# Performance work log

Measured on AMD Instinct MI355X. Metric: run time of the kernel, lower is better.

The kernel has to match this reference:

```python
import jax, jax.numpy as jnp
import numpy as np

K = 7  # kernel_size


def _patches(x, k):
    # x: [N, C, H, W] -> [K*K, N, C, H, W]; zero-padded local windows in
    # torch.nn.functional.unfold order (kernel positions row-major).
    N, C, H, W = x.shape
    p = k // 2
    xp = jnp.pad(x, ((0, 0), (0, 0), (p, p), (p, p)))
    return jnp.stack([xp[:, :, i:i + H, j:j + W]
                      for i in range(k) for j in range(k)], axis=0)


def setup_inputs() -> dict:
    key = jax.random.key(0)
    k1, k2 = jax.random.split(key)
    x = jax.random.normal(k1, (4, 128, 80, 80), dtype=jnp.float32)
    feat_in = jax.random.normal(k2, (4, 128, 80, 80), dtype=jnp.float32)
    return {"x": x, "feat_in": feat_in}


def reference(x, feat_in):
    N, C, H, W = feat_in.shape
    k2 = K * K
    # theta_x == phi_x == x in the original module.
    phi_p = _patches(x, K)                            # [K2, N, Cq, H, W]
    # local dot products: weight[k, n, h, w] = sum_c phi_window * theta_center
    w = jnp.einsum('knchw,nchw->knhw', phi_p, x)      # [K2, N, H, W]
    # L1-style normalization over the window (plain sum, as in the source)
    w = w / jnp.sum(w, axis=0, keepdims=True)
    feat_p = _patches(feat_in, K)                     # [K2, N, C, H, W]
    out = jnp.einsum('knhw,knchw->nchw', w, feat_p)   # [N, C, H, W]
    pairwise_weight = w.transpose(1, 2, 3, 0).reshape(N * H * W, 1, k2)
    return out, pairwise_weight
```

## Files before the change

kernel.cpp:

```cpp
#include <hip/hip_runtime.h>


namespace {

constexpr int CN = 4, CC = 128, HT = 80, WD = 80;
constexpr int KK = 7, K2 = 49, PD = 3;
constexpr int TW = 16, TH = 4;
constexpr int HW_ = TW + 6;
constexpr int HH_ = TH + 6;
constexpr int HENT = HW_ * HH_;
constexpr int HCHUNK = (HENT * 4 + 63) / 64;
constexpr int HPADF = HCHUNK * 64;
constexpr int PLANE = HT * WD;
constexpr int GSTRIDE = 4 * PLANE;
constexpr int OUT_ELEMS = CN * CC * PLANE;
constexpr int NW = 4;
constexpr int GPW = 8;
constexpr int WR = 53;

__device__ __forceinline__ void make_off(int* off, int bx, int by, int lane) {
#pragma unroll
  for (int q = 0; q < HCHUNK; ++q) {
    int f = q * 64 + lane;
    int e = f >> 2;
    if (e > HENT - 1) e = HENT - 1;
    const int ch = f & 3;
    const int r  = e / HW_;
    const int cl = e - r * HW_;
    int gh = by * TH - PD + r;
    gh = gh < 0 ? 0 : (gh > HT - 1 ? HT - 1 : gh);
    int gw = bx * TW - PD + cl;
    gw = gw < 0 ? 0 : (gw > WD - 1 ? WD - 1 : gw);
    off[q] = ch * PLANE + gh * WD + gw;
  }
}

__device__ __forceinline__ void issue_chunks(const float* gbase, const int* off,
                                             float* lds) {
#if __has_builtin(__builtin_amdgcn_global_load_lds)
#pragma unroll
  for (int q = 0; q < HCHUNK; ++q) {
    __builtin_amdgcn_global_load_lds(
        (const __attribute__((address_space(1))) void*)(gbase + off[q]),
        (__attribute__((address_space(3))) void*)(lds + q * 64), 4, 0, 0);
  }
#else
  const int lane = (int)(threadIdx.x & 63);
#pragma unroll
  for (int q = 0; q < HCHUNK; ++q) lds[q * 64 + lane] = gbase[off[q]];
  asm volatile("s_waitcnt lgkmcnt(0)" ::: "memory");
#endif
}

#define WAIT_VM(n_lit)                                      \
  asm volatile("s_waitcnt vmcnt(" #n_lit ")" ::: "memory"); \
  __builtin_amdgcn_sched_barrier(0)

__global__ __launch_bounds__(256) void lnl2d_fused4(
    const float* __restrict__ x, const float* __restrict__ feat,
    float* __restrict__ dout) {
  __shared__ float halo[NW * 3][HPADF];
  __shared__ float wred[64][WR];
  __shared__ float inv[64];

  const int tid  = (int)threadIdx.x;
  const int wv   = tid >> 6;
  const int lane = tid & 63;
  const int tx = lane & (TW - 1), ty = lane >> 4;
  const int bx = (int)blockIdx.x, by = (int)blockIdx.y, n = (int)blockIdx.z;
  const int h = by * TH + ty, w = bx * TW + tx;

  const float* xw = x + (size_t)n * CC * PLANE + (size_t)wv * 32 * PLANE;
  const float* fw = feat + (size_t)n * CC * PLANE + (size_t)wv * 32 * PLANE;
  float* out = dout;
  float* pw  = dout + OUT_ELEMS;

  int off[HCHUNK];
  make_off(off, bx, by, lane);

#pragma unroll
  for (int i = 0; i < (64 * WR + 255) / 256; ++i) {
    const int idx = i * 256 + tid;
    if (idx < 64 * WR) ((float*)wred)[idx] = 0.f;
  }
  __syncthreads();

  float acc[K2];
#pragma unroll
  for (int k = 0; k < K2; ++k) acc[k] = 0.f;

  float* hb0 = halo[wv * 3 + 0];
  float* hb1 = halo[wv * 3 + 1];
  float* hb2 = halo[wv * 3 + 2];

  issue_chunks(xw, off, hb0);
  issue_chunks(xw + GSTRIDE, off, hb1);
  int goff = 2 * GSTRIDE;
#pragma unroll
  for (int g = 0; g < GPW; ++g) {
    if (g < GPW - 2) {
      float* dst = (g % 3 == 0) ? hb2 : ((g % 3 == 1) ? hb0 : hb1);
      issue_chunks(xw + goff, off, dst);
      goff += GSTRIDE;
    }
    if (g < GPW - 2)      { WAIT_VM(28); }
    else if (g == GPW - 2){ WAIT_VM(14); }
    else                  { WAIT_VM(0); }
    const float* hb = (g % 3 == 0) ? hb0 : ((g % 3 == 1) ? hb1 : hb2);
    const float4 c4 = *(const float4*)(hb + ((ty + PD) * HW_ + (tx + PD)) * 4);
#pragma unroll
    for (int di = 0; di < KK; ++di)
#pragma unroll
      for (int dj = 0; dj < KK; ++dj) {
        const float4 n4 = *(const float4*)(hb + ((ty + di) * HW_ + (tx + dj)) * 4);
        acc[di * KK + dj] += c4.x * n4.x + c4.y * n4.y + c4.z * n4.z + c4.w * n4.w;
      }
  }

#pragma unroll
  for (int di = 0; di < KK; ++di)
#pragma unroll
    for (int dj = 0; dj < KK; ++dj) {
      const int hh = h + di - PD, ww = w + dj - PD;
      if ((unsigned)hh >= (unsigned)HT || (unsigned)ww >= (unsigned)WD)
        acc[di * KK + dj] = 0.f;
    }
#pragma unroll
  for (int k = 0; k < K2; ++k) atomicAdd(&wred[lane][k], acc[k]);

  __syncthreads();

  issue_chunks(fw, off, hb0);
  issue_chunks(fw + GSTRIDE, off, hb1);

  float wk[K2];
  float ssum = 0.f;
#pragma unroll
  for (int k = 0; k < K2; ++k) { wk[k] = wred[lane][k]; ssum += wk[k]; }
  const float invs = 1.0f / ssum;
#pragma unroll
  for (int k = 0; k < K2; ++k) wk[k] *= invs;
  if (wv == 0) inv[lane] = invs;

  float4 ov[GPW];
#pragma unroll
  for (int g = 0; g < GPW; ++g) ov[g] = make_float4(0.f, 0.f, 0.f, 0.f);

  goff = 2 * GSTRIDE;
#pragma unroll
  for (int g = 0; g < GPW; ++g) {
    if (g < GPW - 2) {
      float* dst = (g % 3 == 0) ? hb2 : ((g % 3 == 1) ? hb0 : hb1);
      issue_chunks(fw + goff, off, dst);
      goff += GSTRIDE;
    }
    if (g < GPW - 2)      { WAIT_VM(28); }
    else if (g == GPW - 2){ WAIT_VM(14); }
    else                  { WAIT_VM(0); }
    const float* hb = (g % 3 == 0) ? hb0 : ((g % 3 == 1) ? hb1 : hb2);
#pragma unroll
    for (int di = 0; di < KK; ++di)
#pragma unroll
      for (int dj = 0; dj < KK; ++dj) {
        const float4 n4 = *(const float4*)(hb + ((ty + di) * HW_ + (tx + dj)) * 4);
        const float f = wk[di * KK + dj];
        ov[g].x += f * n4.x; ov[g].y += f * n4.y; ov[g].z += f * n4.z; ov[g].w += f * n4.w;
      }
  }

  const size_t ob = (size_t)n * CC * PLANE + (size_t)wv * 32 * PLANE +
                    (size_t)(h * WD + w);
#pragma unroll
  for (int g = 0; g < GPW; ++g) {
    out[ob + (size_t)(4 * g + 0) * PLANE] = ov[g].x;
    out[ob + (size_t)(4 * g + 1) * PLANE] = ov[g].y;
    out[ob + (size_t)(4 * g + 2) * PLANE] = ov[g].z;
    out[ob + (size_t)(4 * g + 3) * PLANE] = ov[g].w;
  }

  __syncthreads();

#pragma unroll
  for (int r = 0; r < TH; ++r) {
    float* seg = pw + (size_t)(n * PLANE + (by * TH + r) * WD + bx * TW) * K2;
#pragma unroll
    for (int i = 0; i < (TW * K2) / 256; ++i) {
      const int idx = i * 256 + tid;
      const int col = idx / K2, k = idx - col * K2;
      seg[idx] = wred[r * TW + col][k] * inv[r * TW + col];
    }
    const int rem = TW * K2 - 256 * ((TW * K2) / 256);
    if (tid < rem) {
      const int idx = 256 * ((TW * K2) / 256) + tid;
      const int col = idx / K2, k = idx - col * K2;
      seg[idx] = wred[r * TW + col][k] * inv[r * TW + col];
    }
  }
}

}

extern "C" void kernel_launch(void* const* d_in, const int* in_sizes, int n_in,
                              void* d_out, int out_size, void* d_ws, size_t ws_size,
                              hipStream_t stream) {
  const float* x    = (const float*)d_in[0];
  const float* feat = (const float*)d_in[1];
  float* out        = (float*)d_out;
  dim3 grid(WD / TW, HT / TH, CN);
  lnl2d_fused4<<<grid, 256, 0, stream>>>(x, feat, out);
}
```

Measured before the change: 137.9 us.

## Split channels across eight waves with register-staged double-buffered halo loads

```diff
diff --git a/kernel.cpp b/kernel.cpp
--- a/kernel.cpp
+++ b/kernel.cpp
@@ -7,59 +7,18 @@
 constexpr int KK = 7, K2 = 49, PD = 3;
 constexpr int TW = 16, TH = 4;
 constexpr int HW_ = TW + 6;
-constexpr int HH_ = TH + 6;
-constexpr int HENT = HW_ * HH_;
-constexpr int HCHUNK = (HENT * 4 + 63) / 64;
-constexpr int HPADF = HCHUNK * 64;
+constexpr int HENT = 22 * 10;
 constexpr int PLANE = HT * WD;
 constexpr int GSTRIDE = 4 * PLANE;
 constexpr int OUT_ELEMS = CN * CC * PLANE;
-constexpr int NW = 4;
-constexpr int GPW = 8;
+constexpr int NW = 8;
+constexpr int GPW = 4;
 constexpr int WR = 53;
 
-__device__ __forceinline__ void make_off(int* off, int bx, int by, int lane) {
-#pragma unroll
-  for (int q = 0; q < HCHUNK; ++q) {
-    int f = q * 64 + lane;
-    int e = f >> 2;
-    if (e > HENT - 1) e = HENT - 1;
-    const int ch = f & 3;
-    const int r  = e / HW_;
-    const int cl = e - r * HW_;
-    int gh = by * TH - PD + r;
-    gh = gh < 0 ? 0 : (gh > HT - 1 ? HT - 1 : gh);
-    int gw = bx * TW - PD + cl;
-    gw = gw < 0 ? 0 : (gw > WD - 1 ? WD - 1 : gw);
-    off[q] = ch * PLANE + gh * WD + gw;
-  }
-}
-
-__device__ __forceinline__ void issue_chunks(const float* gbase, const int* off,
-                                             float* lds) {
-#if __has_builtin(__builtin_amdgcn_global_load_lds)
-#pragma unroll
-  for (int q = 0; q < HCHUNK; ++q) {
-    __builtin_amdgcn_global_load_lds(
-        (const __attribute__((address_space(1))) void*)(gbase + off[q]),
-        (__attribute__((address_space(3))) void*)(lds + q * 64), 4, 0, 0);
-  }
-#else
-  const int lane = (int)(threadIdx.x & 63);
-#pragma unroll
-  for (int q = 0; q < HCHUNK; ++q) lds[q * 64 + lane] = gbase[off[q]];
-  asm volatile("s_waitcnt lgkmcnt(0)" ::: "memory");
-#endif
-}
-
-#define WAIT_VM(n_lit)                                      \
-  asm volatile("s_waitcnt vmcnt(" #n_lit ")" ::: "memory"); \
-  __builtin_amdgcn_sched_barrier(0)
-
-__global__ __launch_bounds__(256) void lnl2d_fused4(
-    const float* __restrict__ x, const float* __restrict__ feat,
-    float* __restrict__ dout) {
-  __shared__ float halo[NW * 3][HPADF];
+__global__ __launch_bounds__(512) void lnl2d_v4(const float* __restrict__ x,
+                                                const float* __restrict__ feat,
+                                                float* __restrict__ dout) {
+  __shared__ float4 halo[NW][256];
   __shared__ float wred[64][WR];
   __shared__ float inv[64];
 
@@ -70,51 +29,71 @@
   const int bx = (int)blockIdx.x, by = (int)blockIdx.y, n = (int)blockIdx.z;
   const int h = by * TH + ty, w = bx * TW + tx;
 
-  const float* xw = x + (size_t)n * CC * PLANE + (size_t)wv * 32 * PLANE;
-  const float* fw = feat + (size_t)n * CC * PLANE + (size_t)wv * 32 * PLANE;
+  const float* xw = x + (size_t)n * CC * PLANE + (size_t)wv * 16 * PLANE;
+  const float* fw = feat + (size_t)n * CC * PLANE + (size_t)wv * 16 * PLANE;
   float* out = dout;
   float* pw  = dout + OUT_ELEMS;
 
-  int off[HCHUNK];
-  make_off(off, bx, by, lane);
+  int off4[4];
+  int eclamp[4];
+#pragma unroll
+  for (int c = 0; c < 4; ++c) {
+    int e = c * 64 + lane;
+    if (e > HENT - 1) e = HENT - 1;
+    eclamp[c] = e;
+    const int r = e / HW_, cl = e - r * HW_;
+    int gh = by * TH - PD + r;
+    gh = gh < 0 ? 0 : (gh > HT - 1 ? HT - 1 : gh);
+    int gw = bx * TW - PD + cl;
+    gw = gw < 0 ? 0 : (gw > WD - 1 ? WD - 1 : gw);
+    off4[c] = gh * WD + gw;
+  }
 
 #pragma unroll
-  for (int i = 0; i < (64 * WR + 255) / 256; ++i) {
-    const int idx = i * 256 + tid;
+  for (int i = 0; i < (64 * WR + 511) / 512; ++i) {
+    const int idx = i * 512 + tid;
     if (idx < 64 * WR) ((float*)wred)[idx] = 0.f;
   }
   __syncthreads();
+
+  auto ldg = [&](const float* gbase, float (&s)[16]) {
+#pragma unroll
+    for (int p = 0; p < 4; ++p) {
+      const float* bp = gbase + p * PLANE;
+#pragma unroll
+      for (int c = 0; c < 4; ++c) s[p * 4 + c] = bp[off4[c]];
+    }
+  };
+  auto stw = [&](const float (&s)[16]) {
+#pragma unroll
+    for (int c = 0; c < 4; ++c)
+      halo[wv][eclamp[c]] = make_float4(s[0 * 4 + c], s[1 * 4 + c],
+                                        s[2 * 4 + c], s[3 * 4 + c]);
+  };
 
   float acc[K2];
 #pragma unroll
   for (int k = 0; k < K2; ++k) acc[k] = 0.f;
 
-  float* hb0 = halo[wv * 3 + 0];
-  float* hb1 = halo[wv * 3 + 1];
-  float* hb2 = halo[wv * 3 + 2];
-
-  issue_chunks(xw, off, hb0);
-  issue_chunks(xw + GSTRIDE, off, hb1);
-  int goff = 2 * GSTRIDE;
-#pragma unroll
-  for (int g = 0; g < GPW; ++g) {
-    if (g < GPW - 2) {
-      float* dst = (g % 3 == 0) ? hb2 : ((g % 3 == 1) ? hb0 : hb1);
-      issue_chunks(xw + goff, off, dst);
-      goff += GSTRIDE;
-    }
-    if (g < GPW - 2)      { WAIT_VM(28); }
-    else if (g == GPW - 2){ WAIT_VM(14); }
-    else                  { WAIT_VM(0); }
-    const float* hb = (g % 3 == 0) ? hb0 : ((g % 3 == 1) ? hb1 : hb2);
-    const float4 c4 = *(const float4*)(hb + ((ty + PD) * HW_ + (tx + PD)) * 4);
+  auto corr = [&]() {
+    const float4 c4 = halo[wv][(ty + PD) * HW_ + (tx + PD)];
 #pragma unroll
     for (int di = 0; di < KK; ++di)
 #pragma unroll
       for (int dj = 0; dj < KK; ++dj) {
-        const float4 n4 = *(const float4*)(hb + ((ty + di) * HW_ + (tx + dj)) * 4);
+        const float4 n4 = halo[wv][(ty + di) * HW_ + (tx + dj)];
         acc[di * KK + dj] += c4.x * n4.x + c4.y * n4.y + c4.z * n4.z + c4.w * n4.w;
       }
+  };
+
+  {
+    float sA[16], sB[16];
+    ldg(xw + 0 * GSTRIDE, sA);
+    ldg(xw + 1 * GSTRIDE, sB);
+    stw(sA); ldg(xw + 2 * GSTRIDE, sA); corr();
+    stw(sB); ldg(xw + 3 * GSTRIDE, sB); corr();
+    stw(sA); corr();
+    stw(sB); corr();
   }
 
 #pragma unroll
@@ -130,8 +109,9 @@
 
   __syncthreads();
 
-  issue_chunks(fw, off, hb0);
-  issue_chunks(fw + GSTRIDE, off, hb1);
+  float sA[16], sB[16];
+  ldg(fw + 0 * GSTRIDE, sA);
+  ldg(fw + 1 * GSTRIDE, sB);
 
   float wk[K2];
   float ssum = 0.f;
@@ -146,29 +126,23 @@
 #pragma unroll
   for (int g = 0; g < GPW; ++g) ov[g] = make_float4(0.f, 0.f, 0.f, 0.f);
 
-  goff = 2 * GSTRIDE;
-#pragma unroll
-  for (int g = 0; g < GPW; ++g) {
-    if (g < GPW - 2) {
-      float* dst = (g % 3 == 0) ? hb2 : ((g % 3 == 1) ? hb0 : hb1);
-      issue_chunks(fw + goff, off, dst);
-      goff += GSTRIDE;
-    }
-    if (g < GPW - 2)      { WAIT_VM(28); }
-    else if (g == GPW - 2){ WAIT_VM(14); }
-    else                  { WAIT_VM(0); }
-    const float* hb = (g % 3 == 0) ? hb0 : ((g % 3 == 1) ? hb1 : hb2);
+  auto agg = [&](float4& o) {
 #pragma unroll
     for (int di = 0; di < KK; ++di)
 #pragma unroll
       for (int dj = 0; dj < KK; ++dj) {
-        const float4 n4 = *(const float4*)(hb + ((ty + di) * HW_ + (tx + dj)) * 4);
+        const float4 n4 = halo[wv][(ty + di) * HW_ + (tx + dj)];
         const float f = wk[di * KK + dj];
-        ov[g].x += f * n4.x; ov[g].y += f * n4.y; ov[g].z += f * n4.z; ov[g].w += f * n4.w;
+        o.x += f * n4.x; o.y += f * n4.y; o.z += f * n4.z; o.w += f * n4.w;
       }
-  }
+  };
 
-  const size_t ob = (size_t)n * CC * PLANE + (size_t)wv * 32 * PLANE +
+  stw(sA); ldg(fw + 2 * GSTRIDE, sA); agg(ov[0]);
+  stw(sB); ldg(fw + 3 * GSTRIDE, sB); agg(ov[1]);
+  stw(sA); agg(ov[2]);
+  stw(sB); agg(ov[3]);
+
+  const size_t ob = (size_t)n * CC * PLANE + (size_t)wv * 16 * PLANE +
                     (size_t)(h * WD + w);
 #pragma unroll
   for (int g = 0; g < GPW; ++g) {
@@ -183,17 +157,15 @@
 #pragma unroll
   for (int r = 0; r < TH; ++r) {
     float* seg = pw + (size_t)(n * PLANE + (by * TH + r) * WD + bx * TW) * K2;
-#pragma unroll
-    for (int i = 0; i < (TW * K2) / 256; ++i) {
-      const int idx = i * 256 + tid;
+    {
+      const int idx = tid;
       const int col = idx / K2, k = idx - col * K2;
       seg[idx] = wred[r * TW + col][k] * inv[r * TW + col];
     }
-    const int rem = TW * K2 - 256 * ((TW * K2) / 256);
-    if (tid < rem) {
-      const int idx = 256 * ((TW * K2) / 256) + tid;
-      const int col = idx / K2, k = idx - col * K2;
-      seg[idx] = wred[r * TW + col][k] * inv[r * TW + col];
+    const int idx2 = 512 + tid;
+    if (idx2 < TW * K2) {
+      const int col = idx2 / K2, k = idx2 - col * K2;
+      seg[idx2] = wred[r * TW + col][k] * inv[r * TW + col];
     }
   }
 }
@@ -207,5 +179,5 @@
   const float* feat = (const float*)d_in[1];
   float* out        = (float*)d_out;
   dim3 grid(WD / TW, HT / TH, CN);
-  lnl2d_fused4<<<grid, 256, 0, stream>>>(x, feat, out);
+  lnl2d_v4<<<grid, 512, 0, stream>>>(x, feat, out);
 }
```

Result: slower. 172.4 us (+25.0%).

## Deepen halo prefetch to four buffers and pad halo row stride

Applied to the files above, without the earlier changes.

```diff
diff --git a/kernel.cpp b/kernel.cpp
--- a/kernel.cpp
+++ b/kernel.cpp
@@ -6,16 +6,14 @@
 constexpr int CN = 4, CC = 128, HT = 80, WD = 80;
 constexpr int KK = 7, K2 = 49, PD = 3;
 constexpr int TW = 16, TH = 4;
-constexpr int HW_ = TW + 6;
-constexpr int HH_ = TH + 6;
-constexpr int HENT = HW_ * HH_;
+constexpr int HROW = 23;
+constexpr int HENT = 10 * HROW;
 constexpr int HCHUNK = (HENT * 4 + 63) / 64;
 constexpr int HPADF = HCHUNK * 64;
 constexpr int PLANE = HT * WD;
 constexpr int GSTRIDE = 4 * PLANE;
 constexpr int OUT_ELEMS = CN * CC * PLANE;
-constexpr int NW = 4;
-constexpr int GPW = 8;
+constexpr int NW = 4, GPW = 8;
 constexpr int WR = 53;
 
 __device__ __forceinline__ void make_off(int* off, int bx, int by, int lane) {
@@ -25,8 +23,8 @@
     int e = f >> 2;
     if (e > HENT - 1) e = HENT - 1;
     const int ch = f & 3;
-    const int r  = e / HW_;
-    const int cl = e - r * HW_;
+    const int r  = e / HROW;
+    const int cl = e - r * HROW;
     int gh = by * TH - PD + r;
     gh = gh < 0 ? 0 : (gh > HT - 1 ? HT - 1 : gh);
     int gw = bx * TW - PD + cl;
@@ -56,10 +54,10 @@
   asm volatile("s_waitcnt vmcnt(" #n_lit ")" ::: "memory"); \
   __builtin_amdgcn_sched_barrier(0)
 
-__global__ __launch_bounds__(256) void lnl2d_fused4(
-    const float* __restrict__ x, const float* __restrict__ feat,
-    float* __restrict__ dout) {
-  __shared__ float halo[NW * 3][HPADF];
+__global__ __launch_bounds__(256) void lnl2d_v6(const float* __restrict__ x,
+                                                const float* __restrict__ feat,
+                                                float* __restrict__ dout) {
+  __shared__ float halo[NW * 4][HPADF];
   __shared__ float wred[64][WR];
   __shared__ float inv[64];
 
@@ -85,36 +83,36 @@
   }
   __syncthreads();
 
+  float* hb[4] = {halo[wv * 4 + 0], halo[wv * 4 + 1], halo[wv * 4 + 2],
+                  halo[wv * 4 + 3]};
+
   float acc[K2];
 #pragma unroll
   for (int k = 0; k < K2; ++k) acc[k] = 0.f;
 
-  float* hb0 = halo[wv * 3 + 0];
-  float* hb1 = halo[wv * 3 + 1];
-  float* hb2 = halo[wv * 3 + 2];
-
-  issue_chunks(xw, off, hb0);
-  issue_chunks(xw + GSTRIDE, off, hb1);
-  int goff = 2 * GSTRIDE;
-#pragma unroll
-  for (int g = 0; g < GPW; ++g) {
-    if (g < GPW - 2) {
-      float* dst = (g % 3 == 0) ? hb2 : ((g % 3 == 1) ? hb0 : hb1);
-      issue_chunks(xw + goff, off, dst);
-      goff += GSTRIDE;
-    }
-    if (g < GPW - 2)      { WAIT_VM(28); }
-    else if (g == GPW - 2){ WAIT_VM(14); }
-    else                  { WAIT_VM(0); }
-    const float* hb = (g % 3 == 0) ? hb0 : ((g % 3 == 1) ? hb1 : hb2);
-    const float4 c4 = *(const float4*)(hb + ((ty + PD) * HW_ + (tx + PD)) * 4);
+  auto corr = [&](const float* b) {
+    const float4* h4 = (const float4*)b;
+    const float4 c4 = h4[(ty + PD) * HROW + tx + PD];
 #pragma unroll
     for (int di = 0; di < KK; ++di)
 #pragma unroll
       for (int dj = 0; dj < KK; ++dj) {
-        const float4 n4 = *(const float4*)(hb + ((ty + di) * HW_ + (tx + dj)) * 4);
+        const float4 n4 = h4[(ty + di) * HROW + tx + dj];
         acc[di * KK + dj] += c4.x * n4.x + c4.y * n4.y + c4.z * n4.z + c4.w * n4.w;
       }
+  };
+
+  issue_chunks(xw + 0 * GSTRIDE, off, hb[0]);
+  issue_chunks(xw + 1 * GSTRIDE, off, hb[1]);
+  issue_chunks(xw + 2 * GSTRIDE, off, hb[2]);
+#pragma unroll
+  for (int g = 0; g < GPW; ++g) {
+    if (g < GPW - 3) issue_chunks(xw + (g + 3) * GSTRIDE, off, hb[(g + 3) & 3]);
+    if (g < GPW - 3)      { WAIT_VM(45); }
+    else if (g == GPW - 3){ WAIT_VM(30); }
+    else if (g == GPW - 2){ WAIT_VM(15); }
+    else                  { WAIT_VM(0); }
+    corr(hb[g & 3]);
   }
 
 #pragma unroll
@@ -130,8 +128,9 @@
 
   __syncthreads();
 
-  issue_chunks(fw, off, hb0);
-  issue_chunks(fw + GSTRIDE, off, hb1);
+  issue_chunks(fw + 0 * GSTRIDE, off, hb[0]);
+  issue_chunks(fw + 1 * GSTRIDE, off, hb[1]);
+  issue_chunks(fw + 2 * GSTRIDE, off, hb[2]);
 
   float wk[K2];
   float ssum = 0.f;
@@ -146,23 +145,19 @@
 #pragma unroll
   for (int g = 0; g < GPW; ++g) ov[g] = make_float4(0.f, 0.f, 0.f, 0.f);
 
-  goff = 2 * GSTRIDE;
 #pragma unroll
   for (int g = 0; g < GPW; ++g) {
-    if (g < GPW - 2) {
-      float* dst = (g % 3 == 0) ? hb2 : ((g % 3 == 1) ? hb0 : hb1);
-      issue_chunks(fw + goff, off, dst);
-      goff += GSTRIDE;
-    }
-    if (g < GPW - 2)      { WAIT_VM(28); }
-    else if (g == GPW - 2){ WAIT_VM(14); }
+    if (g < GPW - 3) issue_chunks(fw + (g + 3) * GSTRIDE, off, hb[(g + 3) & 3]);
+    if (g < GPW - 3)      { WAIT_VM(45); }
+    else if (g == GPW - 3){ WAIT_VM(30); }
+    else if (g == GPW - 2){ WAIT_VM(15); }
     else                  { WAIT_VM(0); }
-    const float* hb = (g % 3 == 0) ? hb0 : ((g % 3 == 1) ? hb1 : hb2);
+    const float4* h4 = (const float4*)hb[g & 3];
 #pragma unroll
     for (int di = 0; di < KK; ++di)
 #pragma unroll
       for (int dj = 0; dj < KK; ++dj) {
-        const float4 n4 = *(const float4*)(hb + ((ty + di) * HW_ + (tx + dj)) * 4);
+        const float4 n4 = h4[(ty + di) * HROW + tx + dj];
         const float f = wk[di * KK + dj];
         ov[g].x += f * n4.x; ov[g].y += f * n4.y; ov[g].z += f * n4.z; ov[g].w += f * n4.w;
       }
@@ -207,5 +202,5 @@
   const float* feat = (const float*)d_in[1];
   float* out        = (float*)d_out;
   dim3 grid(WD / TW, HT / TH, CN);
-  lnl2d_fused4<<<grid, 256, 0, stream>>>(x, feat, out);
-}
+  lnl2d_v6<<<grid, 256, 0, stream>>>(x, feat, out);
+}
```

Result: no change. 137.7 us (-0.2%).
